# Kernel optimization log

Hardware: AMD Instinct MI355X
Metric: run time of the kernel (lower is better)

The kernel has to match this reference:

```python
import jax, jax.numpy as jnp
import numpy as np

B, T, F, H = 128, 512, 256, 512


def setup_inputs() -> dict:
    key = jax.random.key(0)
    k1, k2, k3, k4 = jax.random.split(key, 4)
    scale_k = 1.0 / np.sqrt(F)
    scale_r = 1.0 / np.sqrt(H)
    return {
        "x": jax.random.normal(k1, (B, T, F), dtype=jnp.float32),
        "kernel": jax.random.normal(k2, (F, 4 * H), dtype=jnp.float32) * scale_k,
        "recurrent_kernel": jax.random.normal(k3, (H, 4 * H), dtype=jnp.float32) * scale_r,
        "bias": jax.random.normal(k4, (4 * H,), dtype=jnp.float32) * 0.01,
    }


def _lstm(x, kernel, recurrent_kernel, bias):
    # x: [B, T, F] -> scan over time. Keras gate order: i, f, g(cell), o.
    h0 = jnp.zeros((x.shape[0], H), dtype=x.dtype)
    c0 = jnp.zeros((x.shape[0], H), dtype=x.dtype)
    # Precompute input projections for all timesteps in one big GEMM: [B,T,4H]
    xz = jnp.einsum('btf,fg->btg', x, kernel) + bias

    def step(carry, xz_t):
        h, c = carry
        z = xz_t + h @ recurrent_kernel  # [B, 4H]
        i, f, g, o = jnp.split(z, 4, axis=-1)
        i = jax.nn.sigmoid(i)
        f = jax.nn.sigmoid(f)
        g = jnp.tanh(g)
        o = jax.nn.sigmoid(o)
        c_new = f * c + i * g
        h_new = o * jnp.tanh(c_new)
        return (h_new, c_new), h_new

    (h_last, c_last), hs = jax.lax.scan(step, (h0, c0), jnp.swapaxes(xz, 0, 1))
    output = jnp.swapaxes(hs, 0, 1)  # [B, T, H]
    return output, h_last, c_last


def reference(x, kernel, recurrent_kernel, bias):
    # Inference-mode forward (dropout inactive), matching Keras LSTM eval behavior.
    output, h, c = _lstm(x, kernel, recurrent_kernel, bias)
    return (output, h, c)
```

## Files before the change

### kernel.cpp

```cpp
#include <hip/hip_runtime.h>
#include <stdint.h>


#define Bb 128
#define Tt 512
#define Ff 256
#define Hh 512
#define G4 2048

typedef __attribute__((ext_vector_type(8))) short short8;
typedef __attribute__((ext_vector_type(4))) float floatx4;
typedef __attribute__((ext_vector_type(4))) unsigned int uint4v;

__device__ __forceinline__ unsigned short f2bf(float f) {
    unsigned u = __float_as_uint(f);
    return (unsigned short)((u + 0x7FFFu + ((u >> 16) & 1u)) >> 16);
}
__device__ __forceinline__ float bf2f(unsigned short h) {
    return __uint_as_float(((unsigned)h) << 16);
}
__device__ __forceinline__ float sigm(float x) { return 1.f / (1.f + __expf(-x)); }
__device__ __forceinline__ float tanh_f(float x) {
    float e = __expf(-2.f * fabsf(x));
    return copysignf((1.f - e) / (1.f + e), x);
}

__global__ __launch_bounds__(256, 2) void lstm_xz(
    const float* __restrict__ x, const float* __restrict__ w,
    const float* __restrict__ bias, _Float16* __restrict__ xzh)
{
    __shared__ unsigned short Ahi[128 * 40];
    __shared__ unsigned short Alo[128 * 40];
    __shared__ unsigned short Wt [128 * 40];

    const int tid = threadIdx.x;
    int idx = blockIdx.x;
    int xcd = idx & 7;
    int chunk = idx >> 3;
    int msup = chunk >> 7;
    int s = chunk & 127;
    int nt = s >> 3;
    int mi0 = s & 7;
    int mt = xcd * 64 + msup * 8 + mi0;
    const int m0 = mt << 7;
    const int n0 = nt << 7;

    const int lane = tid & 63;
    const int wv = tid >> 6;
    const int wm = wv >> 1, wn = wv & 1;
    const int cB = lane & 15, kgrp = lane >> 4;

    floatx4 acc[4][4];
#pragma unroll
    for (int i = 0; i < 4; ++i)
#pragma unroll
        for (int j = 0; j < 4; ++j) acc[i][j] = (floatx4){0.f, 0.f, 0.f, 0.f};

    float bv[4];
#pragma unroll
    for (int ni = 0; ni < 4; ++ni) bv[ni] = bias[n0 + wn * 64 + ni * 16 + cB];

    for (int it = 0; it < 8; ++it) {
        const int k0 = it * 32;
#pragma unroll
        for (int sw = 0; sw < 4; ++sw) {
            int e = sw * 256 + tid;
            int row = e >> 3, kq = e & 7;
            float4 v = *((const float4*)(x + (size_t)(m0 + row) * Ff + k0) + kq);
            unsigned short h0 = f2bf(v.x), h1 = f2bf(v.y), h2 = f2bf(v.z), h3 = f2bf(v.w);
            unsigned short l0 = f2bf(v.x - bf2f(h0)), l1 = f2bf(v.y - bf2f(h1));
            unsigned short l2 = f2bf(v.z - bf2f(h2)), l3 = f2bf(v.w - bf2f(h3));
            uint2 ph, pl;
            ph.x = (unsigned)h0 | ((unsigned)h1 << 16); ph.y = (unsigned)h2 | ((unsigned)h3 << 16);
            pl.x = (unsigned)l0 | ((unsigned)l1 << 16); pl.y = (unsigned)l2 | ((unsigned)l3 << 16);
            *(uint2*)(&Ahi[row * 40 + kq * 4]) = ph;
            *(uint2*)(&Alo[row * 40 + kq * 4]) = pl;
        }
#pragma unroll
        for (int sw = 0; sw < 4; ++sw) {
            int e = sw * 256 + tid;
            int kr = e >> 5, nq = e & 31;
            float4 v = *((const float4*)(w + (size_t)(k0 + kr) * G4 + n0) + nq);
            int nb = nq * 4;
            Wt[(nb + 0) * 40 + kr] = f2bf(v.x);
            Wt[(nb + 1) * 40 + kr] = f2bf(v.y);
            Wt[(nb + 2) * 40 + kr] = f2bf(v.z);
            Wt[(nb + 3) * 40 + kr] = f2bf(v.w);
        }
        __syncthreads();

        short8 bfr[4];
#pragma unroll
        for (int ni = 0; ni < 4; ++ni)
            bfr[ni] = *(const short8*)(&Wt[(wn * 64 + ni * 16 + cB) * 40 + kgrp * 8]);
#pragma unroll
        for (int mi = 0; mi < 4; ++mi) {
            short8 ah = *(const short8*)(&Ahi[(wm * 64 + mi * 16 + cB) * 40 + kgrp * 8]);
            short8 al = *(const short8*)(&Alo[(wm * 64 + mi * 16 + cB) * 40 + kgrp * 8]);
#pragma unroll
            for (int ni = 0; ni < 4; ++ni) {
                acc[mi][ni] = __builtin_amdgcn_mfma_f32_16x16x32_bf16(ah, bfr[ni], acc[mi][ni], 0, 0, 0);
                acc[mi][ni] = __builtin_amdgcn_mfma_f32_16x16x32_bf16(al, bfr[ni], acc[mi][ni], 0, 0, 0);
            }
        }
        __syncthreads();
    }
#pragma unroll
    for (int mi = 0; mi < 4; ++mi)
#pragma unroll
        for (int ni = 0; ni < 4; ++ni) {
            int rowb = m0 + wm * 64 + mi * 16 + kgrp * 4;
            int col = n0 + wn * 64 + ni * 16 + cB;
#pragma unroll
            for (int rr = 0; rr < 4; ++rr)
                xzh[(size_t)(rowb + rr) * G4 + col] = (_Float16)(acc[mi][ni][rr] + bv[ni]);
        }
}

__global__ __launch_bounds__(256, 1) void lstm_rec(
    const _Float16* __restrict__ xzh, const float* __restrict__ rk,
    unsigned* __restrict__ hbuf_u, unsigned* __restrict__ bar,
    float* __restrict__ out)
{
    __shared__ unsigned short Rlds[128 * 512];
    __shared__ unsigned short hlds[16 * 512];

    const int tid = threadIdx.x;
    const int idx = blockIdx.x;
    const int rg = idx & 7;
    const int cb = idx >> 3;
    const int b0 = rg * 16;
    const int hc0 = cb * 32;

    const int lane = tid & 63;
    const int wv = tid >> 6;
    const int cB = lane & 15, kgrp = lane >> 4;
    const int hcw = hc0 + wv * 8;
    const int c7 = cB & 7;
    const int col = hcw + c7;
    const bool hi = (cB & 8) != 0;

    for (int e = tid; e < 64 * 512; e += 256) {
        int p = e & 63, k = e >> 6;
        int n0 = 2 * p;
        int loc = n0 & 31, w = n0 >> 5;
        int gate = ((loc >> 4) << 1) | ((loc >> 3) & 1);
        int gcol = gate * Hh + hc0 + w * 8 + (loc & 7);
        float2 v = *(const float2*)(rk + (size_t)k * G4 + gcol);
        Rlds[n0 * 512 + (k ^ ((n0 & 7) << 3))] = f2bf(v.x);
        Rlds[(n0 + 1) * 512 + (k ^ (((n0 + 1) & 7) << 3))] = f2bf(v.y);
    }

    unsigned* hb0 = hbuf_u;
    unsigned* hb1 = hbuf_u + (size_t)Bb * Hh / 2;
    unsigned* flags = bar + rg * 64;

    float creg[4] = {0.f, 0.f, 0.f, 0.f};
    float xzr[16];
    const unsigned* xz_u = (const unsigned*)xzh;

    const unsigned* pxz[16];
#pragma unroll
    for (int g = 0; g < 4; ++g)
#pragma unroll
        for (int r = 0; r < 4; ++r) {
            size_t b = (size_t)(b0 + kgrp * 4 + r);
            pxz[g * 4 + r] = xz_u + ((b * Tt) * G4 + (size_t)g * Hh + (col & ~1)) / 2;
        }

#pragma unroll
    for (int i = 0; i < 16; ++i) {
        unsigned v = pxz[i][0];
        xzr[i] = (float)__builtin_bit_cast(_Float16,
            (unsigned short)((col & 1) ? (v >> 16) : (v & 0xffffu)));
    }
    __syncthreads();

    unsigned* hlds_u = (unsigned*)hlds;
    const int skip_lo = cb * 4, skip_hi = cb * 4 + 3;

    for (int t = 0; t < Tt; ++t) {
        const bool last = (t == Tt - 1);
        const unsigned* hrd = (t & 1) ? hb1 : hb0;
        unsigned* hwr = (t & 1) ? hb0 : hb1;

        unsigned pf[16];
        if (!last) {
#pragma unroll
            for (int i = 0; i < 16; ++i) pf[i] = pxz[i][(size_t)(t + 1) * (G4 / 2)];
        }

        if (t > 0) {
            const unsigned tgt = (unsigned)t;
            for (;;) {
                unsigned f = tgt;
                if (lane < skip_lo || lane > skip_hi)
                    f = __hip_atomic_load(flags + lane, __ATOMIC_RELAXED,
                                          __HIP_MEMORY_SCOPE_AGENT);
                if (__all(f >= tgt)) break;
            }
        }

        {
            const unsigned* hbr = hrd + (size_t)b0 * 256;
            const unsigned* p0 = hbr + (wv + 0) * 256 + 4 * lane;
            const unsigned* p1 = hbr + (wv + 4) * 256 + 4 * lane;
            const unsigned* p2 = hbr + (wv + 8) * 256 + 4 * lane;
            const unsigned* p3 = hbr + (wv + 12) * 256 + 4 * lane;
            uint4v t0, t1, t2, t3;
            asm volatile("global_load_dwordx4 %0, %1, off sc0 sc1" : "=v"(t0) : "v"(p0) : "memory");
            asm volatile("global_load_dwordx4 %0, %1, off sc0 sc1" : "=v"(t1) : "v"(p1) : "memory");
            asm volatile("global_load_dwordx4 %0, %1, off sc0 sc1" : "=v"(t2) : "v"(p2) : "memory");
            asm volatile("global_load_dwordx4 %0, %1, off sc0 sc1" : "=v"(t3) : "v"(p3) : "memory");
            asm volatile("s_waitcnt vmcnt(0)" ::: "memory");
            __builtin_amdgcn_sched_barrier(0);
            *(uint4v*)(hlds_u + (wv + 0) * 256 + 4 * (lane ^ ((wv + 0) & 7))) = t0;
            *(uint4v*)(hlds_u + (wv + 4) * 256 + 4 * (lane ^ ((wv + 4) & 7))) = t1;
            *(uint4v*)(hlds_u + (wv + 8) * 256 + 4 * (lane ^ ((wv + 8) & 7))) = t2;
            *(uint4v*)(hlds_u + (wv + 12) * 256 + 4 * (lane ^ ((wv + 12) & 7))) = t3;
        }
        __syncthreads();

        floatx4 acc0 = (floatx4){0.f, 0.f, 0.f, 0.f};
        floatx4 acc1 = (floatx4){0.f, 0.f, 0.f, 0.f};
        {
            const int nb = wv * 32;
            const int swz = (cB & 7) << 3;
#pragma unroll
            for (int kk = 0; kk < 16; ++kk) {
                int kb = (kk * 32 + kgrp * 8) ^ swz;
                short8 a   = *(const short8*)&hlds[cB * 512 + kb];
                short8 bb0 = *(const short8*)&Rlds[(nb + cB) * 512 + kb];
                short8 bb1 = *(const short8*)&Rlds[(nb + 16 + cB) * 512 + kb];
                acc0 = __builtin_amdgcn_mfma_f32_16x16x32_bf16(a, bb0, acc0, 0, 0, 0);
                acc1 = __builtin_amdgcn_mfma_f32_16x16x32_bf16(a, bb1, acc1, 0, 0, 0);
            }
        }

        float hv[4];
#pragma unroll
        for (int r = 0; r < 4; ++r) {
            float a0 = acc0[r], a1 = acc1[r];
            float a0x = __shfl_xor(a0, 8);
            float a1x = __shfl_xor(a1, 8);
            float zi = (hi ? a0x : a0) + xzr[0 * 4 + r];
            float zf = (hi ? a0 : a0x) + xzr[1 * 4 + r];
            float zg = (hi ? a1x : a1) + xzr[2 * 4 + r];
            float zo = (hi ? a1 : a1x) + xzr[3 * 4 + r];
            creg[r] = sigm(zf) * creg[r] + sigm(zi) * tanh_f(zg);
            hv[r] = sigm(zo) * tanh_f(creg[r]);
        }

        float hn[4];
#pragma unroll
        for (int r = 0; r < 4; ++r) hn[r] = __shfl_xor(hv[r], 1);
        const bool ew = (!hi && !(cB & 1));

        if (!last) {
#pragma unroll
            for (int r = 0; r < 4; ++r) {
                if (ew) {
                    size_t b = (size_t)(b0 + kgrp * 4 + r);
                    unsigned hp = (unsigned)f2bf(hv[r]) | ((unsigned)f2bf(hn[r]) << 16);
                    __hip_atomic_store(hwr + b * 256 + (col >> 1), hp,
                                       __ATOMIC_RELAXED, __HIP_MEMORY_SCOPE_AGENT);
                }
            }
            asm volatile("s_waitcnt vmcnt(0)" ::: "memory");
            if (lane == 0)
                __hip_atomic_store(flags + cb * 4 + wv, (unsigned)(t + 1),
                                   __ATOMIC_RELAXED, __HIP_MEMORY_SCOPE_AGENT);
        }

#pragma unroll
        for (int r = 0; r < 4; ++r) {
            if (ew) {
                size_t b = (size_t)(b0 + kgrp * 4 + r);
                *(float2*)(out + (b * Tt + (size_t)t) * Hh + col) = make_float2(hv[r], hn[r]);
            }
        }

        if (last) {
            float* hl = out + (size_t)Bb * Tt * Hh;
            float* cl = hl + (size_t)Bb * Hh;
#pragma unroll
            for (int r = 0; r < 4; ++r) {
                float cn = __shfl_xor(creg[r], 1);
                if (ew) {
                    size_t b = (size_t)(b0 + kgrp * 4 + r);
                    *(float2*)(hl + b * Hh + col) = make_float2(hv[r], hn[r]);
                    *(float2*)(cl + b * Hh + col) = make_float2(creg[r], cn);
                }
            }
            break;
        }

#pragma unroll
        for (int i = 0; i < 16; ++i)
            xzr[i] = (float)__builtin_bit_cast(_Float16,
                (unsigned short)((col & 1) ? (pf[i] >> 16) : (pf[i] & 0xffffu)));

        __syncthreads();
    }
}

extern "C" void kernel_launch(void* const* d_in, const int* in_sizes, int n_in,
                              void* d_out, int out_size, void* d_ws, size_t ws_size,
                              hipStream_t stream) {
    (void)in_sizes; (void)n_in; (void)out_size; (void)ws_size;
    const float* x    = (const float*)d_in[0];
    const float* w    = (const float*)d_in[1];
    const float* rk   = (const float*)d_in[2];
    const float* bias = (const float*)d_in[3];
    float* out = (float*)d_out;

    char* ws = (char*)d_ws;
    const size_t XZ_BYTES   = (size_t)Bb * Tt * G4 * sizeof(_Float16);
    const size_t HBUF_BYTES = (size_t)2 * Bb * Hh * sizeof(unsigned short);
    const size_t BAR_BYTES  = 2048;

    _Float16* xzh = (_Float16*)ws;
    unsigned* hbuf = (unsigned*)(ws + XZ_BYTES);
    unsigned* bar = (unsigned*)(ws + XZ_BYTES + HBUF_BYTES);

    hipMemsetAsync(ws + XZ_BYTES, 0, HBUF_BYTES + BAR_BYTES, stream);

    lstm_xz<<<dim3(8192), dim3(256), 0, stream>>>(x, w, bias, xzh);
    lstm_rec<<<dim3(128), dim3(256), 0, stream>>>(xzh, rk, hbuf, bar, out);
}
```

Measured before the change: 2.526 ms.

## Replace flag barrier with sentinel-tagged 4-slot ring buffer for hidden state exchange

```diff
diff --git a/kernel.cpp b/kernel.cpp
--- a/kernel.cpp
+++ b/kernel.cpp
@@ -7,6 +7,7 @@
 #define Ff 256
 #define Hh 512
 #define G4 2048
+#define SENT 0xFFFFFFFFu
 
 typedef __attribute__((ext_vector_type(8))) short short8;
 typedef __attribute__((ext_vector_type(4))) float floatx4;
@@ -119,8 +120,7 @@
 
 __global__ __launch_bounds__(256, 1) void lstm_rec(
     const _Float16* __restrict__ xzh, const float* __restrict__ rk,
-    unsigned* __restrict__ hbuf_u, unsigned* __restrict__ bar,
-    float* __restrict__ out)
+    unsigned* __restrict__ hbuf_u, float* __restrict__ out)
 {
     __shared__ unsigned short Rlds[128 * 512];
     __shared__ unsigned short hlds[16 * 512];
@@ -151,89 +151,96 @@
         Rlds[(n0 + 1) * 512 + (k ^ (((n0 + 1) & 7) << 3))] = f2bf(v.y);
     }
 
-    unsigned* hb0 = hbuf_u;
-    unsigned* hb1 = hbuf_u + (size_t)Bb * Hh / 2;
-    unsigned* flags = bar + rg * 64;
+    const unsigned* xz_u = (const unsigned*)xzh;
+    const unsigned* pr[4];
+#pragma unroll
+    for (int r = 0; r < 4; ++r)
+        pr[r] = xz_u + ((size_t)(b0 + kgrp * 4 + r) * Tt * G4 + (col & ~1)) / 2;
+
+    float xzr[16];
+#pragma unroll
+    for (int g = 0; g < 4; ++g)
+#pragma unroll
+        for (int r = 0; r < 4; ++r) {
+            unsigned v = pr[r][g * 256];
+            xzr[g * 4 + r] = (float)__builtin_bit_cast(_Float16,
+                (unsigned short)((col & 1) ? (v >> 16) : (v & 0xffffu)));
+        }
+#pragma unroll
+    for (int r = 0; r < 4; ++r) pr[r] += G4 / 2;
+
+    __syncthreads();
+
+    short8 bf0[16], bf1[16];
+    {
+        const int nb = wv * 32;
+        const int swz = c7 << 3;
+#pragma unroll
+        for (int kk = 0; kk < 16; ++kk) {
+            int kb = (kk * 32 + kgrp * 8) ^ swz;
+            bf0[kk] = *(const short8*)&Rlds[(nb + cB) * 512 + kb];
+            bf1[kk] = *(const short8*)&Rlds[(nb + 16 + cB) * 512 + kb];
+        }
+    }
 
     float creg[4] = {0.f, 0.f, 0.f, 0.f};
-    float xzr[16];
-    const unsigned* xz_u = (const unsigned*)xzh;
-
-    const unsigned* pxz[16];
-#pragma unroll
-    for (int g = 0; g < 4; ++g)
-#pragma unroll
-        for (int r = 0; r < 4; ++r) {
-            size_t b = (size_t)(b0 + kgrp * 4 + r);
-            pxz[g * 4 + r] = xz_u + ((b * Tt) * G4 + (size_t)g * Hh + (col & ~1)) / 2;
-        }
-
-#pragma unroll
-    for (int i = 0; i < 16; ++i) {
-        unsigned v = pxz[i][0];
-        xzr[i] = (float)__builtin_bit_cast(_Float16,
-            (unsigned short)((col & 1) ? (v >> 16) : (v & 0xffffu)));
-    }
-    __syncthreads();
-
     unsigned* hlds_u = (unsigned*)hlds;
-    const int skip_lo = cb * 4, skip_hi = cb * 4 + 3;
+    unsigned* const gbase = hbuf_u + (size_t)rg * 4 * 4096;
 
     for (int t = 0; t < Tt; ++t) {
         const bool last = (t == Tt - 1);
-        const unsigned* hrd = (t & 1) ? hb1 : hb0;
-        unsigned* hwr = (t & 1) ? hb0 : hb1;
 
         unsigned pf[16];
         if (!last) {
 #pragma unroll
-            for (int i = 0; i < 16; ++i) pf[i] = pxz[i][(size_t)(t + 1) * (G4 / 2)];
-        }
-
-        if (t > 0) {
-            const unsigned tgt = (unsigned)t;
-            for (;;) {
-                unsigned f = tgt;
-                if (lane < skip_lo || lane > skip_hi)
-                    f = __hip_atomic_load(flags + lane, __ATOMIC_RELAXED,
-                                          __HIP_MEMORY_SCOPE_AGENT);
-                if (__all(f >= tgt)) break;
-            }
-        }
-
-        {
-            const unsigned* hbr = hrd + (size_t)b0 * 256;
-            const unsigned* p0 = hbr + (wv + 0) * 256 + 4 * lane;
-            const unsigned* p1 = hbr + (wv + 4) * 256 + 4 * lane;
-            const unsigned* p2 = hbr + (wv + 8) * 256 + 4 * lane;
-            const unsigned* p3 = hbr + (wv + 12) * 256 + 4 * lane;
-            uint4v t0, t1, t2, t3;
-            asm volatile("global_load_dwordx4 %0, %1, off sc0 sc1" : "=v"(t0) : "v"(p0) : "memory");
-            asm volatile("global_load_dwordx4 %0, %1, off sc0 sc1" : "=v"(t1) : "v"(p1) : "memory");
-            asm volatile("global_load_dwordx4 %0, %1, off sc0 sc1" : "=v"(t2) : "v"(p2) : "memory");
-            asm volatile("global_load_dwordx4 %0, %1, off sc0 sc1" : "=v"(t3) : "v"(p3) : "memory");
-            asm volatile("s_waitcnt vmcnt(0)" ::: "memory");
-            __builtin_amdgcn_sched_barrier(0);
-            *(uint4v*)(hlds_u + (wv + 0) * 256 + 4 * (lane ^ ((wv + 0) & 7))) = t0;
-            *(uint4v*)(hlds_u + (wv + 4) * 256 + 4 * (lane ^ ((wv + 4) & 7))) = t1;
-            *(uint4v*)(hlds_u + (wv + 8) * 256 + 4 * (lane ^ ((wv + 8) & 7))) = t2;
-            *(uint4v*)(hlds_u + (wv + 12) * 256 + 4 * (lane ^ ((wv + 12) & 7))) = t3;
-        }
-        __syncthreads();
+            for (int g = 0; g < 4; ++g)
+#pragma unroll
+                for (int r = 0; r < 4; ++r)
+                    pf[g * 4 + r] = pr[r][g * 256];
+        }
 
         floatx4 acc0 = (floatx4){0.f, 0.f, 0.f, 0.f};
         floatx4 acc1 = (floatx4){0.f, 0.f, 0.f, 0.f};
-        {
-            const int nb = wv * 32;
-            const int swz = (cB & 7) << 3;
+
+        if (t > 0) {
+            const unsigned* sb = gbase + ((t - 1) & 3) * 4096;
+            const unsigned* p0 = sb + (wv + 0) * 256 + 4 * lane;
+            const unsigned* p1 = sb + (wv + 4) * 256 + 4 * lane;
+            const unsigned* p2 = sb + (wv + 8) * 256 + 4 * lane;
+            const unsigned* p3 = sb + (wv + 12) * 256 + 4 * lane;
+            uint4v v0, v1, v2, v3;
+            for (;;) {
+                asm volatile("global_load_dwordx4 %0, %1, off sc0 sc1" : "=v"(v0) : "v"(p0) : "memory");
+                asm volatile("global_load_dwordx4 %0, %1, off sc0 sc1" : "=v"(v1) : "v"(p1) : "memory");
+                asm volatile("global_load_dwordx4 %0, %1, off sc0 sc1" : "=v"(v2) : "v"(p2) : "memory");
+                asm volatile("global_load_dwordx4 %0, %1, off sc0 sc1" : "=v"(v3) : "v"(p3) : "memory");
+                asm volatile("s_waitcnt vmcnt(0)" ::: "memory");
+                bool bad = (v0[0] == SENT) | (v0[1] == SENT) | (v0[2] == SENT) | (v0[3] == SENT)
+                         | (v1[0] == SENT) | (v1[1] == SENT) | (v1[2] == SENT) | (v1[3] == SENT)
+                         | (v2[0] == SENT) | (v2[1] == SENT) | (v2[2] == SENT) | (v2[3] == SENT)
+                         | (v3[0] == SENT) | (v3[1] == SENT) | (v3[2] == SENT) | (v3[3] == SENT);
+                if (!bad) break;
+            }
+            __builtin_amdgcn_sched_barrier(0);
+            *(uint4v*)(hlds_u + (wv + 0) * 256 + 4 * (lane ^ ((wv + 0) & 7))) = v0;
+            *(uint4v*)(hlds_u + (wv + 4) * 256 + 4 * (lane ^ ((wv + 4) & 7))) = v1;
+            *(uint4v*)(hlds_u + (wv + 8) * 256 + 4 * (lane ^ ((wv + 8) & 7))) = v2;
+            *(uint4v*)(hlds_u + (wv + 12) * 256 + 4 * (lane ^ ((wv + 12) & 7))) = v3;
+            __syncthreads();
+
+            if (t >= 2) {
+                unsigned* rs = gbase + ((t - 2) & 3) * 4096
+                             + (tid >> 4) * 256 + (hc0 >> 1) + (tid & 15);
+                __hip_atomic_store(rs, SENT, __ATOMIC_RELAXED, __HIP_MEMORY_SCOPE_AGENT);
+            }
+
+            const int swz = c7 << 3;
 #pragma unroll
             for (int kk = 0; kk < 16; ++kk) {
                 int kb = (kk * 32 + kgrp * 8) ^ swz;
-                short8 a   = *(const short8*)&hlds[cB * 512 + kb];
-                short8 bb0 = *(const short8*)&Rlds[(nb + cB) * 512 + kb];
-                short8 bb1 = *(const short8*)&Rlds[(nb + 16 + cB) * 512 + kb];
-                acc0 = __builtin_amdgcn_mfma_f32_16x16x32_bf16(a, bb0, acc0, 0, 0, 0);
-                acc1 = __builtin_amdgcn_mfma_f32_16x16x32_bf16(a, bb1, acc1, 0, 0, 0);
+                short8 a = *(const short8*)&hlds[cB * 512 + kb];
+                acc0 = __builtin_amdgcn_mfma_f32_16x16x32_bf16(a, bf0[kk], acc0, 0, 0, 0);
+                acc1 = __builtin_amdgcn_mfma_f32_16x16x32_bf16(a, bf1[kk], acc1, 0, 0, 0);
             }
         }
 
@@ -257,19 +264,15 @@
         const bool ew = (!hi && !(cB & 1));
 
         if (!last) {
+            unsigned* wbase = gbase + (t & 3) * 4096;
 #pragma unroll
             for (int r = 0; r < 4; ++r) {
                 if (ew) {
-                    size_t b = (size_t)(b0 + kgrp * 4 + r);
                     unsigned hp = (unsigned)f2bf(hv[r]) | ((unsigned)f2bf(hn[r]) << 16);
-                    __hip_atomic_store(hwr + b * 256 + (col >> 1), hp,
+                    __hip_atomic_store(wbase + (kgrp * 4 + r) * 256 + (col >> 1), hp,
                                        __ATOMIC_RELAXED, __HIP_MEMORY_SCOPE_AGENT);
                 }
             }
-            asm volatile("s_waitcnt vmcnt(0)" ::: "memory");
-            if (lane == 0)
-                __hip_atomic_store(flags + cb * 4 + wv, (unsigned)(t + 1),
-                                   __ATOMIC_RELAXED, __HIP_MEMORY_SCOPE_AGENT);
         }
 
 #pragma unroll
@@ -299,6 +302,8 @@
         for (int i = 0; i < 16; ++i)
             xzr[i] = (float)__builtin_bit_cast(_Float16,
                 (unsigned short)((col & 1) ? (pf[i] >> 16) : (pf[i] & 0xffffu)));
+#pragma unroll
+        for (int r = 0; r < 4; ++r) pr[r] += G4 / 2;
 
         __syncthreads();
     }
@@ -316,15 +321,13 @@
 
     char* ws = (char*)d_ws;
     const size_t XZ_BYTES   = (size_t)Bb * Tt * G4 * sizeof(_Float16);
-    const size_t HBUF_BYTES = (size_t)2 * Bb * Hh * sizeof(unsigned short);
-    const size_t BAR_BYTES  = 2048;
+    const size_t HBUF_BYTES = (size_t)8 * 4 * 16 * 256 * 4;
 
     _Float16* xzh = (_Float16*)ws;
     unsigned* hbuf = (unsigned*)(ws + XZ_BYTES);
-    unsigned* bar = (unsigned*)(ws + XZ_BYTES + HBUF_BYTES);
-
-    hipMemsetAsync(ws + XZ_BYTES, 0, HBUF_BYTES + BAR_BYTES, stream);
+
+    hipMemsetAsync(ws + XZ_BYTES, 0xFF, HBUF_BYTES, stream);
 
     lstm_xz<<<dim3(8192), dim3(256), 0, stream>>>(x, w, bias, xzh);
-    lstm_rec<<<dim3(128), dim3(256), 0, stream>>>(xzh, rk, hbuf, bar, out);
-}
+    lstm_rec<<<dim3(128), dim3(256), 0, stream>>>(xzh, rk, hbuf, out);
+}
```

Measured after the change: 2.203 ms. 12.8% less time.
